# Performance work log

Hardware: AMD Instinct MI355X
Metric: run time of the kernel (lower is better)

## Reference

```python
import jax, jax.numpy as jnp
import numpy as np

# ---- quantization constants (8-bit, per-tensor affine; representative values) ----
Q_MAX = 255.0
S_IN, Z_IN = 0.05, 128.0      # block input
S1, Z1 = 0.04, 128.0          # after expand 1x1 + hardswish
S2, Z2 = 0.04, 128.0          # after depthwise 5x5 + hardswish
S_SE1, Z_SE1 = 0.03, 128.0    # SE fc1 output
S_SE2, Z_SE2 = 1.0 / 255.0, 0.0  # SE fc2 hardsigmoid output in [0,1]
S_MUL, Z_MUL = 0.04, 128.0    # SE gated activation
S3, Z3 = 0.05, 128.0          # after project 1x1
S_OUT, Z_OUT = 0.06, 128.0    # after residual add
W_SCALE = 0.01                # symmetric per-tensor weight scale (zero_point = 0)
EXP_C = 576                   # expanded channels (depthwise groups)


def conv(x, w, stride=1, padding=0, groups=1):
    return jax.lax.conv_general_dilated(
        x, w, (stride, stride), [(padding, padding), (padding, padding)],
        feature_group_count=groups, dimension_numbers=('NCHW', 'OIHW', 'NCHW'))


def hardswish(x):
    return x * jnp.clip(x + 3.0, 0.0, 6.0) * (1.0 / 6.0)


def hardsigmoid(x):
    return jnp.clip(x + 3.0, 0.0, 6.0) * (1.0 / 6.0)


def qconv(x_q, w_q, b_q, s_in, z_in, s_out, z_out, stride=1, padding=0, groups=1, act=None):
    """Quantized conv: int-domain accumulation (simulated in fp32), fused activation
    on the dequantized accumulator, then requantize to [0, Q_MAX]."""
    acc = conv(x_q - z_in, w_q, stride, padding, groups) + b_q[None, :, None, None]
    deq = acc * (s_in * W_SCALE)  # dequantize accumulator
    if act == 'hardswish':
        deq = hardswish(deq)
    elif act == 'hardsigmoid':
        deq = hardsigmoid(deq)
    return jnp.clip(deq * (1.0 / s_out) + z_out, 0.0, Q_MAX)


def setup_inputs() -> dict:
    key = jax.random.key(0)
    ks = jax.random.split(key, 11)
    def qw(k, shape):  # int8-style symmetric weights stored as fp32 integers
        return jnp.round(jnp.clip(jax.random.normal(k, shape) * 40.0, -127.0, 127.0))
    def qb(k, n):      # int32-style bias in accumulator domain
        return jnp.round(jax.random.normal(k, (n,)) * 500.0)
    return {
        'x':      jnp.round(jax.random.uniform(ks[0], (64, 96, 28, 28)) * Q_MAX),
        'w_exp':  qw(ks[1], (576, 96, 1, 1)),  'b_exp':  qb(ks[2], 576),
        'w_dw':   qw(ks[3], (576, 1, 5, 5)),   'b_dw':   qb(ks[4], 576),
        'w_se1':  qw(ks[5], (144, 576, 1, 1)), 'b_se1':  qb(ks[6], 144),
        'w_se2':  qw(ks[7], (576, 144, 1, 1)), 'b_se2':  qb(ks[8], 576),
        'w_proj': qw(ks[9], (96, 576, 1, 1)),  'b_proj': qb(ks[10], 96),
    }


def reference(x, w_exp, b_exp, w_dw, b_dw, w_se1, b_se1, w_se2, b_se2, w_proj, b_proj):
    # expand 1x1 (+ hardswish)
    e = qconv(x, w_exp, b_exp, S_IN, Z_IN, S1, Z1, act='hardswish')
    # depthwise 5x5, padding=(5-1)//2=2, groups=expanded (+ hardswish)
    d = qconv(e, w_dw, b_dw, S1, Z1, S2, Z2, padding=2, groups=EXP_C, act='hardswish')
    # squeeze-excitation: global avg pool -> fc1 -> fc2(hardsigmoid) -> quantized mul
    pooled = jnp.mean(d, axis=(2, 3), keepdims=True)  # [N, 576, 1, 1]
    g1 = qconv(pooled, w_se1, b_se1, S2, Z2, S_SE1, Z_SE1)
    g2 = qconv(g1, w_se2, b_se2, S_SE1, Z_SE1, S_SE2, Z_SE2, act='hardsigmoid')
    gated = jnp.clip((g2 - Z_SE2) * (d - Z2) * (S_SE2 * S2 / S_MUL) + Z_MUL, 0.0, Q_MAX)
    # project 1x1 (linear)
    p = qconv(gated, w_proj, b_proj, S_MUL, Z_MUL, S3, Z3)
    # quantized residual add (stride=1, in==out channels -> use_res_connect)
    out = jnp.clip((x - Z_IN) * (S_IN / S_OUT) + (p - Z3) * (S3 / S_OUT) + Z_OUT, 0.0, Q_MAX)
    return out
```

## Files before the change

### kernel.cpp

```cpp
#include <hip/hip_runtime.h>

typedef _Float16 v8h __attribute__((ext_vector_type(8)));
typedef _Float16 v4h __attribute__((ext_vector_type(4)));
typedef _Float16 v4h_a4 __attribute__((ext_vector_type(4), aligned(4)));
typedef _Float16 v2h __attribute__((ext_vector_type(2)));
typedef float v4f __attribute__((ext_vector_type(4)));

#define NB 64
#define CI 96
#define CE 576
#define CO 96
#define HW 784
#define SEC 144

#if defined(__has_builtin)
#if __has_builtin(__builtin_amdgcn_fdot2)
#define HAVE_FDOT2 1
#endif
#endif

__device__ __forceinline__ float fdot2(v2h a, v2h b, float c) {
#ifdef HAVE_FDOT2
  return __builtin_amdgcn_fdot2(a, b, c, false);
#else
  return (float)a[0] * (float)b[0] + ((float)a[1] * (float)b[1] + c);
#endif
}

__global__ __launch_bounds__(256) void k0_cvt_w(const float* __restrict__ w_exp,
                                                const float* __restrict__ w_proj,
                                                _Float16* __restrict__ w_exp_h,
                                                _Float16* __restrict__ w_proj_h) {
  int i = blockIdx.x * 256 + threadIdx.x;
  if (i < CE * CI) {
    w_exp_h[i]  = (_Float16)w_exp[i];
    w_proj_h[i] = (_Float16)w_proj[i];
  }
}

__global__ __launch_bounds__(256) void k0x_pack(const float* __restrict__ x,
                                                _Float16* __restrict__ x_f) {
  __shared__ _Float16 xl[112][104];
  const int tid = threadIdx.x;
  const int n = blockIdx.y;
  const int hw0 = blockIdx.x * 112;

  for (int idx = tid; idx < CI * 28; idx += 256) {
    int c = idx / 28, seg = idx % 28;
    const float4 v = *(const float4*)&x[(n * CI + c) * HW + hw0 + seg * 4];
    int row = seg * 4;
    xl[row + 0][c] = (_Float16)(v.x - 128.0f);
    xl[row + 1][c] = (_Float16)(v.y - 128.0f);
    xl[row + 2][c] = (_Float16)(v.z - 128.0f);
    xl[row + 3][c] = (_Float16)(v.w - 128.0f);
  }
  __syncthreads();

  for (int idx = tid; idx < 1344; idx += 256) {
    int t_l = idx / 192, rem = idx % 192, s = rem / 64, ln = rem % 64;
    int hw_l = t_l * 16 + (ln & 15), ci = s * 32 + (ln >> 4) * 8;
    v8h o;
#pragma unroll
    for (int j = 0; j < 8; ++j) o[j] = xl[hw_l][ci + j];
    size_t t = (size_t)(blockIdx.x * 7 + t_l);
    *(v8h*)&x_f[(((size_t)n * 49 + t) * 3 + s) * 512 + ln * 8] = o;
  }
}

__global__ __launch_bounds__(512, 4) void k12_fused(const _Float16* __restrict__ x_f,
                                                    const _Float16* __restrict__ w_exp_h,
                                                    const float* __restrict__ b_exp,
                                                    const float* __restrict__ w_dw,
                                                    const float* __restrict__ b_dw,
                                                    _Float16* __restrict__ d_t,
                                                    float* __restrict__ d_sums) {
  __shared__ _Float16 e_lds[16][32][36];
  __shared__ _Float16 d_tile[16][784];
  __shared__ _Float16 w_pairs[16][5][8];
  const int tid = threadIdx.x;
  const int n = blockIdx.y;
  const int c0 = blockIdx.x * 16;

  {
    unsigned long long* z = (unsigned long long*)&e_lds[0][0][0];
    for (int idx = tid; idx < 16 * 32 * 36 * 2 / 8; idx += 512) z[idx] = 0ull;
  }
  for (int idx = tid; idx < 640; idx += 512) {
    int c = idx / 40, r = idx % 40, dy = r / 8, k = r % 8;
    int tap = (k < 4) ? k : (k - 3);
    w_pairs[c][dy][k] = (_Float16)w_dw[(c0 + c) * 25 + dy * 5 + tap];
  }
  __syncthreads();

  const int wv = tid >> 6, lane = tid & 63;
  const int l15 = lane & 15, q = lane >> 4;

  {
    const _Float16* wrow = &w_exp_h[(c0 + l15) * CI + q * 8];
    v8h a0 = *(const v8h*)(wrow);
    v8h a1 = *(const v8h*)(wrow + 32);
    v8h a2 = *(const v8h*)(wrow + 64);
    float bia[4];
#pragma unroll
    for (int r = 0; r < 4; ++r) bia[r] = b_exp[c0 + q * 4 + r];

    const _Float16* xb = x_f + (size_t)n * (49 * 3 * 512) + lane * 8;
    for (int t = wv; t < 49; t += 8) {
      const _Float16* xt = xb + (size_t)t * (3 * 512);
      v8h b0 = *(const v8h*)(xt);
      v8h b1 = *(const v8h*)(xt + 512);
      v8h b2 = *(const v8h*)(xt + 1024);
      v4f acc = (v4f){0.f, 0.f, 0.f, 0.f};
      acc = __builtin_amdgcn_mfma_f32_16x16x32_f16(a0, b0, acc, 0, 0, 0);
      acc = __builtin_amdgcn_mfma_f32_16x16x32_f16(a1, b1, acc, 0, 0, 0);
      acc = __builtin_amdgcn_mfma_f32_16x16x32_f16(a2, b2, acc, 0, 0, 0);
      int hw = t * 16 + l15;
      int y = hw / 28, xx = hw - y * 28;
#pragma unroll
      for (int r = 0; r < 4; ++r) {
        float deq = (acc[r] + bia[r]) * 5.0e-4f;
        float cl  = fminf(fmaxf(deq + 3.0f, 0.0f), 6.0f);
        float ev  = fminf(fmaxf(deq * cl * (25.0f / 6.0f), -128.0f), 127.0f);
        e_lds[q * 4 + r][2 + y][6 + xx] = (_Float16)ev;
      }
    }
  }
  __syncthreads();

  const int c = tid >> 5, l = tid & 31;
  v2h W01[5], W23[5], W12[5], W34[5];
  float W0s[5], W4s[5];
#pragma unroll
  for (int dy = 0; dy < 5; ++dy) {
    W01[dy] = *(const v2h*)&w_pairs[c][dy][0];
    W23[dy] = *(const v2h*)&w_pairs[c][dy][2];
    W12[dy] = *(const v2h*)&w_pairs[c][dy][4];
    W34[dy] = *(const v2h*)&w_pairs[c][dy][6];
    W0s[dy] = (float)W01[dy][0];
    W4s[dy] = (float)W34[dy][1];
  }
  const float bc = b_dw[c0 + c];

  float csum = 0.0f;
  if (l < 28) {
    const int y = l;
    v2h P0[5], P1[5], P2[5], P3[5];
#pragma unroll
    for (int dy = 0; dy < 5; ++dy) {
      const _Float16* row = &e_lds[c][y + dy][0];
      v4h w01 = *(const v4h*)(row + 4);
      v4h w23 = *(const v4h*)(row + 8);
      P0[dy] = (v2h){w01[0], w01[1]};
      P1[dy] = (v2h){w01[2], w01[3]};
      P2[dy] = (v2h){w23[0], w23[1]};
      P3[dy] = (v2h){w23[2], w23[3]};
    }
#pragma unroll
    for (int x0 = 0; x0 < 28; x0 += 4) {
      float o0 = bc, o1 = bc, o2 = bc, o3 = bc;
#pragma unroll
      for (int dy = 0; dy < 5; ++dy) {
        o0 = fdot2(P0[dy], W01[dy], o0);
        o0 = fdot2(P1[dy], W23[dy], o0);
        o0 += (float)P2[dy][0] * W4s[dy];
        o1 += (float)P0[dy][1] * W0s[dy];
        o1 = fdot2(P1[dy], W12[dy], o1);
        o1 = fdot2(P2[dy], W34[dy], o1);
        o2 = fdot2(P1[dy], W01[dy], o2);
        o2 = fdot2(P2[dy], W23[dy], o2);
        o2 += (float)P3[dy][0] * W4s[dy];
        o3 += (float)P1[dy][1] * W0s[dy];
        o3 = fdot2(P2[dy], W12[dy], o3);
        o3 = fdot2(P3[dy], W34[dy], o3);
      }
      v4h dv;
      float oo[4] = {o0, o1, o2, o3};
#pragma unroll
      for (int i = 0; i < 4; ++i) {
        float deq = oo[i] * 4.0e-4f;
        float cl  = fminf(fmaxf(deq + 3.0f, 0.0f), 6.0f);
        float dvv = fminf(fmaxf(deq * cl * (25.0f / 6.0f), -128.0f), 127.0f);
        dv[i] = (_Float16)dvv;
        csum += dvv;
      }
      *(v4h*)&d_tile[c][y * 28 + x0] = dv;
      if (x0 < 24) {
#pragma unroll
        for (int dy = 0; dy < 5; ++dy) {
          const _Float16* row = &e_lds[c][y + dy][0];
          v4h nw = *(const v4h*)(row + x0 + 12);
          P0[dy] = P2[dy];
          P1[dy] = P3[dy];
          P2[dy] = (v2h){nw[0], nw[1]};
          P3[dy] = (v2h){nw[2], nw[3]};
        }
      }
    }
  }
#pragma unroll
  for (int m = 16; m >= 1; m >>= 1) csum += __shfl_xor(csum, m);
  if (l == 0) d_sums[n * CE + c0 + c] = csum;

  __syncthreads();
  const size_t obase = ((size_t)n * 72 + (c0 >> 3)) * 784;
  for (int hw = tid; hw < 784; hw += 512) {
    v8h o0, o1;
#pragma unroll
    for (int j = 0; j < 8; ++j) { o0[j] = d_tile[j][hw]; o1[j] = d_tile[8 + j][hw]; }
    *(v8h*)&d_t[(obase + hw) * 8] = o0;
    *(v8h*)&d_t[(obase + 784 + hw) * 8] = o1;
  }
}

__global__ __launch_bounds__(256) void k3a_fc1(const float* __restrict__ d_sums,
                                               const float* __restrict__ w_se1,
                                               const float* __restrict__ b_se1,
                                               float* __restrict__ g1) {
  const int tid = threadIdx.x;
  const int wv = tid >> 6, lane = tid & 63;
  const int n = blockIdx.y;
  const int o = blockIdx.x * 4 + wv;
  const float* wrow = &w_se1[o * CE];
  const float* srow = &d_sums[n * CE];
  float p = 0.f;
#pragma unroll
  for (int s = 0; s < 9; ++s) {
    int cc = lane + s * 64;
    p += wrow[cc] * srow[cc];
  }
#pragma unroll
  for (int m = 32; m >= 1; m >>= 1) p += __shfl_xor(p, m);
  if (lane == 0) {
    float deq = (p * (1.0f / 784.0f) + b_se1[o]) * 4.0e-4f;
    g1[n * SEC + o] = fminf(fmaxf(deq * 33.3333333f + 128.0f, 0.0f), 255.0f) - 128.0f;
  }
}

__global__ __launch_bounds__(256) void k3b_fc2(const float* __restrict__ g1,
                                               const float* __restrict__ w_se2,
                                               const float* __restrict__ b_se2,
                                               _Float16* __restrict__ g2h) {
  const int tid = threadIdx.x;
  const int wv = tid >> 6, lane = tid & 63;
  const int n = blockIdx.y;
  const int o = blockIdx.x * 4 + wv;
  const float* wrow = &w_se2[o * SEC];
  const float* grow = &g1[n * SEC];
  float p = wrow[lane] * grow[lane] + wrow[lane + 64] * grow[lane + 64];
  if (lane < 16) p += wrow[lane + 128] * grow[lane + 128];
#pragma unroll
  for (int m = 32; m >= 1; m >>= 1) p += __shfl_xor(p, m);
  if (lane == 0) {
    float deq = (p + b_se2[o]) * 3.0e-4f;
    g2h[n * CE + o] =
        (_Float16)(fminf(fmaxf(deq + 3.0f, 0.0f), 6.0f) * (1.0f / 6.0f));
  }
}

__global__ __launch_bounds__(192) void k4_proj(const _Float16* __restrict__ d_t,
                                               const _Float16* __restrict__ g2h,
                                               const _Float16* __restrict__ w_proj_h,
                                               const float* __restrict__ b_proj,
                                               const float* __restrict__ x,
                                               float* __restrict__ out) {
  const int tid = threadIdx.x;
  const int n = blockIdx.z;
  const int co0 = blockIdx.y * 48;
  const int hw0 = blockIdx.x * 112;
  const int wv = tid >> 6, lane = tid & 63;
  const int l15 = lane & 15, q = lane >> 4;

  v4f acc[7];
#pragma unroll
  for (int t = 0; t < 7; ++t) acc[t] = (v4f){0.f, 0.f, 0.f, 0.f};

  const _Float16* dbase = d_t + (((size_t)n * 72 + q) * 784 + hw0 + l15) * 8;
  const _Float16* abase = &w_proj_h[(co0 + wv * 16 + l15) * CE + q * 8];
  const _Float16* gbase = &g2h[(size_t)n * CE + q * 8];

  for (int ks = 0; ks < 18; ++ks) {
    v8h a = *(const v8h*)(abase + ks * 32);
    v8h g = *(const v8h*)(gbase + ks * 32);
    v8h ag = a * g;
    const _Float16* dk = dbase + (size_t)ks * (4 * 784 * 8);
#pragma unroll
    for (int t = 0; t < 7; ++t) {
      v8h b = *(const v8h*)(dk + t * (16 * 8));
      acc[t] = __builtin_amdgcn_mfma_f32_16x16x32_f16(ag, b, acc[t], 0, 0, 0);
    }
  }

  float bia[4];
#pragma unroll
  for (int r = 0; r < 4; ++r) bia[r] = b_proj[co0 + wv * 16 + q * 4 + r];

#pragma unroll
  for (int t = 0; t < 7; ++t) {
#pragma unroll
    for (int r = 0; r < 4; ++r) {
      int co = co0 + wv * 16 + q * 4 + r;
      int hw = hw0 + t * 16 + l15;
      float p = fminf(fmaxf((acc[t][r] + bia[r]) * 4.0e-4f * 20.0f + 128.0f, 0.0f), 255.0f);
      float xv = x[(n * CO + co) * HW + hw];
      float o = (xv - 128.0f) * 0.8333333333f + (p - 128.0f) * 0.8333333333f + 128.0f;
      out[(n * CO + co) * HW + hw] = fminf(fmaxf(o, 0.0f), 255.0f);
    }
  }
}

extern "C" void kernel_launch(void* const* d_in, const int* in_sizes, int n_in,
                              void* d_out, int out_size, void* d_ws, size_t ws_size,
                              hipStream_t stream) {
  const float* x      = (const float*)d_in[0];
  const float* w_exp  = (const float*)d_in[1];
  const float* b_exp  = (const float*)d_in[2];
  const float* w_dw   = (const float*)d_in[3];
  const float* b_dw   = (const float*)d_in[4];
  const float* w_se1  = (const float*)d_in[5];
  const float* b_se1  = (const float*)d_in[6];
  const float* w_se2  = (const float*)d_in[7];
  const float* b_se2  = (const float*)d_in[8];
  const float* w_proj = (const float*)d_in[9];
  const float* b_proj = (const float*)d_in[10];
  float* out = (float*)d_out;

  char* ws = (char*)d_ws;
  const size_t SZ_W  = (size_t)CE * CI * 2;
  const size_t SZ_XF = (size_t)NB * 49 * 3 * 512 * 2;
  const size_t SZ_D  = (size_t)NB * CE * HW * 2;
  const size_t SZ_S  = (size_t)NB * CE * 4;
  _Float16* w_exp_h  = (_Float16*)(ws);
  _Float16* w_proj_h = (_Float16*)(ws + SZ_W);
  _Float16* x_f      = (_Float16*)(ws + 2 * SZ_W);
  _Float16* d_t      = (_Float16*)(ws + 2 * SZ_W + SZ_XF);
  float*    d_sums   = (float*)   (ws + 2 * SZ_W + SZ_XF + SZ_D);
  float*    g1       = (float*)   (ws + 2 * SZ_W + SZ_XF + SZ_D + SZ_S);
  _Float16* g2h      = (_Float16*)(ws + 2 * SZ_W + SZ_XF + SZ_D + 2 * SZ_S);

  k0_cvt_w<<<(CE * CI + 255) / 256, 256, 0, stream>>>(w_exp, w_proj, w_exp_h, w_proj_h);
  k0x_pack<<<dim3(7, NB), 256, 0, stream>>>(x, x_f);
  k12_fused<<<dim3(36, NB), 512, 0, stream>>>(x_f, w_exp_h, b_exp, w_dw, b_dw, d_t, d_sums);
  k3a_fc1<<<dim3(36, NB), 256, 0, stream>>>(d_sums, w_se1, b_se1, g1);
  k3b_fc2<<<dim3(144, NB), 256, 0, stream>>>(g1, w_se2, b_se2, g2h);
  k4_proj<<<dim3(7, 2, NB), 192, 0, stream>>>(d_t, g2h, w_proj_h, b_proj, x, out);
}
```

Baseline: 179.5 us.

## Split fused expand+depthwise kernel into two spatial halves with halo recompute

The fused expand-1x1 plus depthwise-5x5 kernel now splits each image into two 14-row halves, one per block. Each block recomputes the expand output for a 2-row halo, which the tile loop covers as 28 of the 49 tiles. Smaller LDS tiles and launch bounds raised to 8 blocks/CU aim to double block count and improve occupancy. Per-half channel sums go to a doubled buffer that fc1 adds together. In exchange, about 14% of the expand MFMA work is redundant and the depthwise loop has an irregular tail.

```diff
diff --git a/kernel.cpp b/kernel.cpp
--- a/kernel.cpp
+++ b/kernel.cpp
@@ -2,7 +2,6 @@
 
 typedef _Float16 v8h __attribute__((ext_vector_type(8)));
 typedef _Float16 v4h __attribute__((ext_vector_type(4)));
-typedef _Float16 v4h_a4 __attribute__((ext_vector_type(4), aligned(4)));
 typedef _Float16 v2h __attribute__((ext_vector_type(2)));
 typedef float v4f __attribute__((ext_vector_type(4)));
 
@@ -67,23 +66,24 @@
   }
 }
 
-__global__ __launch_bounds__(512, 4) void k12_fused(const _Float16* __restrict__ x_f,
+__global__ __launch_bounds__(512, 8) void k12_fused(const _Float16* __restrict__ x_f,
                                                     const _Float16* __restrict__ w_exp_h,
                                                     const float* __restrict__ b_exp,
                                                     const float* __restrict__ w_dw,
                                                     const float* __restrict__ b_dw,
                                                     _Float16* __restrict__ d_t,
-                                                    float* __restrict__ d_sums) {
-  __shared__ _Float16 e_lds[16][32][36];
-  __shared__ _Float16 d_tile[16][784];
+                                                    float* __restrict__ d_sums2) {
+  __shared__ _Float16 e_lds[16][18][38];
+  __shared__ _Float16 d_tile[16][392];
   __shared__ _Float16 w_pairs[16][5][8];
   const int tid = threadIdx.x;
-  const int n = blockIdx.y;
+  const int n = blockIdx.z;
+  const int h = blockIdx.y;
   const int c0 = blockIdx.x * 16;
 
   {
     unsigned long long* z = (unsigned long long*)&e_lds[0][0][0];
-    for (int idx = tid; idx < 16 * 32 * 36 * 2 / 8; idx += 512) z[idx] = 0ull;
+    for (int idx = tid; idx < 16 * 18 * 38 * 2 / 8; idx += 512) z[idx] = 0ull;
   }
   for (int idx = tid; idx < 640; idx += 512) {
     int c = idx / 40, r = idx % 40, dy = r / 8, k = r % 8;
@@ -104,8 +104,10 @@
 #pragma unroll
     for (int r = 0; r < 4; ++r) bia[r] = b_exp[c0 + q * 4 + r];
 
+    const int ir0 = 14 * h - 2;
     const _Float16* xb = x_f + (size_t)n * (49 * 3 * 512) + lane * 8;
-    for (int t = wv; t < 49; t += 8) {
+    for (int t_l = wv; t_l < 28; t_l += 8) {
+      int t = 21 * h + t_l;
       const _Float16* xt = xb + (size_t)t * (3 * 512);
       v8h b0 = *(const v8h*)(xt);
       v8h b1 = *(const v8h*)(xt + 512);
@@ -116,12 +118,13 @@
       acc = __builtin_amdgcn_mfma_f32_16x16x32_f16(a2, b2, acc, 0, 0, 0);
       int hw = t * 16 + l15;
       int y = hw / 28, xx = hw - y * 28;
+      int r_l = y - ir0;
 #pragma unroll
       for (int r = 0; r < 4; ++r) {
         float deq = (acc[r] + bia[r]) * 5.0e-4f;
         float cl  = fminf(fmaxf(deq + 3.0f, 0.0f), 6.0f);
         float ev  = fminf(fmaxf(deq * cl * (25.0f / 6.0f), -128.0f), 127.0f);
-        e_lds[q * 4 + r][2 + y][6 + xx] = (_Float16)ev;
+        e_lds[q * 4 + r][r_l][6 + xx] = (_Float16)ev;
       }
     }
   }
@@ -143,20 +146,20 @@
 
   float csum = 0.0f;
   if (l < 28) {
-    const int y = l;
+    const int ry = l >> 1;
+    const int bx = (l & 1) * 14;
     v2h P0[5], P1[5], P2[5], P3[5];
 #pragma unroll
     for (int dy = 0; dy < 5; ++dy) {
-      const _Float16* row = &e_lds[c][y + dy][0];
-      v4h w01 = *(const v4h*)(row + 4);
-      v4h w23 = *(const v4h*)(row + 8);
-      P0[dy] = (v2h){w01[0], w01[1]};
-      P1[dy] = (v2h){w01[2], w01[3]};
-      P2[dy] = (v2h){w23[0], w23[1]};
-      P3[dy] = (v2h){w23[2], w23[3]};
-    }
-#pragma unroll
-    for (int x0 = 0; x0 < 28; x0 += 4) {
+      const _Float16* row = &e_lds[c][ry + dy][bx];
+      P0[dy] = *(const v2h*)(row + 4);
+      P1[dy] = *(const v2h*)(row + 6);
+      P2[dy] = *(const v2h*)(row + 8);
+      P3[dy] = *(const v2h*)(row + 10);
+    }
+#pragma unroll
+    for (int xi = 0; xi < 3; ++xi) {
+      const int x0 = bx + xi * 4;
       float o0 = bc, o1 = bc, o2 = bc, o3 = bc;
 #pragma unroll
       for (int dy = 0; dy < 5; ++dy) {
@@ -173,46 +176,68 @@
         o3 = fdot2(P2[dy], W12[dy], o3);
         o3 = fdot2(P3[dy], W34[dy], o3);
       }
-      v4h dv;
       float oo[4] = {o0, o1, o2, o3};
+      v2h dva, dvb;
 #pragma unroll
       for (int i = 0; i < 4; ++i) {
+        float deq = oo[i] * 4.0e-4f;
+        float cl  = fminf(fmaxf(deq + 3.0f, 0.0f), 6.0f);
+        float dvv = fminf(fmaxf(deq * cl * (25.0f / 6.0f), -128.0f), 127.0f);
+        if (i < 2) dva[i] = (_Float16)dvv; else dvb[i - 2] = (_Float16)dvv;
+        csum += dvv;
+      }
+      *(v2h*)&d_tile[c][ry * 28 + x0]     = dva;
+      *(v2h*)&d_tile[c][ry * 28 + x0 + 2] = dvb;
+#pragma unroll
+      for (int dy = 0; dy < 5; ++dy) {
+        const _Float16* row = &e_lds[c][ry + dy][bx];
+        P0[dy] = P2[dy];
+        P1[dy] = P3[dy];
+        P2[dy] = *(const v2h*)(row + x0 - bx + 12);
+        P3[dy] = *(const v2h*)(row + x0 - bx + 14);
+      }
+    }
+    {
+      float o0 = bc, o1 = bc;
+#pragma unroll
+      for (int dy = 0; dy < 5; ++dy) {
+        o0 = fdot2(P0[dy], W01[dy], o0);
+        o0 = fdot2(P1[dy], W23[dy], o0);
+        o0 += (float)P2[dy][0] * W4s[dy];
+        o1 += (float)P0[dy][1] * W0s[dy];
+        o1 = fdot2(P1[dy], W12[dy], o1);
+        o1 = fdot2(P2[dy], W34[dy], o1);
+      }
+      v2h dv;
+      float oo[2] = {o0, o1};
+#pragma unroll
+      for (int i = 0; i < 2; ++i) {
         float deq = oo[i] * 4.0e-4f;
         float cl  = fminf(fmaxf(deq + 3.0f, 0.0f), 6.0f);
         float dvv = fminf(fmaxf(deq * cl * (25.0f / 6.0f), -128.0f), 127.0f);
         dv[i] = (_Float16)dvv;
         csum += dvv;
       }
-      *(v4h*)&d_tile[c][y * 28 + x0] = dv;
-      if (x0 < 24) {
-#pragma unroll
-        for (int dy = 0; dy < 5; ++dy) {
-          const _Float16* row = &e_lds[c][y + dy][0];
-          v4h nw = *(const v4h*)(row + x0 + 12);
-          P0[dy] = P2[dy];
-          P1[dy] = P3[dy];
-          P2[dy] = (v2h){nw[0], nw[1]};
-          P3[dy] = (v2h){nw[2], nw[3]};
-        }
-      }
+      *(v2h*)&d_tile[c][ry * 28 + bx + 12] = dv;
     }
   }
 #pragma unroll
   for (int m = 16; m >= 1; m >>= 1) csum += __shfl_xor(csum, m);
-  if (l == 0) d_sums[n * CE + c0 + c] = csum;
+  if (l == 0) d_sums2[((size_t)h * NB + n) * CE + c0 + c] = csum;
 
   __syncthreads();
-  const size_t obase = ((size_t)n * 72 + (c0 >> 3)) * 784;
-  for (int hw = tid; hw < 784; hw += 512) {
+  const size_t obase = ((size_t)n * 72 + (c0 >> 3)) * 784 + 392 * h;
+  if (tid < 392) {
+    int hw_l = tid;
     v8h o0, o1;
 #pragma unroll
-    for (int j = 0; j < 8; ++j) { o0[j] = d_tile[j][hw]; o1[j] = d_tile[8 + j][hw]; }
-    *(v8h*)&d_t[(obase + hw) * 8] = o0;
-    *(v8h*)&d_t[(obase + 784 + hw) * 8] = o1;
-  }
-}
-
-__global__ __launch_bounds__(256) void k3a_fc1(const float* __restrict__ d_sums,
+    for (int j = 0; j < 8; ++j) { o0[j] = d_tile[j][hw_l]; o1[j] = d_tile[8 + j][hw_l]; }
+    *(v8h*)&d_t[(obase + hw_l) * 8] = o0;
+    *(v8h*)&d_t[(obase + 784 + hw_l) * 8] = o1;
+  }
+}
+
+__global__ __launch_bounds__(256) void k3a_fc1(const float* __restrict__ d_sums2,
                                                const float* __restrict__ w_se1,
                                                const float* __restrict__ b_se1,
                                                float* __restrict__ g1) {
@@ -221,12 +246,13 @@
   const int n = blockIdx.y;
   const int o = blockIdx.x * 4 + wv;
   const float* wrow = &w_se1[o * CE];
-  const float* srow = &d_sums[n * CE];
+  const float* s0 = &d_sums2[(size_t)n * CE];
+  const float* s1 = &d_sums2[((size_t)NB + n) * CE];
   float p = 0.f;
 #pragma unroll
   for (int s = 0; s < 9; ++s) {
     int cc = lane + s * 64;
-    p += wrow[cc] * srow[cc];
+    p += wrow[cc] * (s0[cc] + s1[cc]);
   }
 #pragma unroll
   for (int m = 32; m >= 1; m >>= 1) p += __shfl_xor(p, m);
@@ -328,19 +354,20 @@
   const size_t SZ_W  = (size_t)CE * CI * 2;
   const size_t SZ_XF = (size_t)NB * 49 * 3 * 512 * 2;
   const size_t SZ_D  = (size_t)NB * CE * HW * 2;
+  const size_t SZ_S2 = (size_t)2 * NB * CE * 4;
   const size_t SZ_S  = (size_t)NB * CE * 4;
   _Float16* w_exp_h  = (_Float16*)(ws);
   _Float16* w_proj_h = (_Float16*)(ws + SZ_W);
   _Float16* x_f      = (_Float16*)(ws + 2 * SZ_W);
   _Float16* d_t      = (_Float16*)(ws + 2 * SZ_W + SZ_XF);
-  float*    d_sums   = (float*)   (ws + 2 * SZ_W + SZ_XF + SZ_D);
-  float*    g1       = (float*)   (ws + 2 * SZ_W + SZ_XF + SZ_D + SZ_S);
-  _Float16* g2h      = (_Float16*)(ws + 2 * SZ_W + SZ_XF + SZ_D + 2 * SZ_S);
+  float*    d_sums2  = (float*)   (ws + 2 * SZ_W + SZ_XF + SZ_D);
+  float*    g1       = (float*)   (ws + 2 * SZ_W + SZ_XF + SZ_D + SZ_S2);
+  _Float16* g2h      = (_Float16*)(ws + 2 * SZ_W + SZ_XF + SZ_D + SZ_S2 + SZ_S);
 
   k0_cvt_w<<<(CE * CI + 255) / 256, 256, 0, stream>>>(w_exp, w_proj, w_exp_h, w_proj_h);
   k0x_pack<<<dim3(7, NB), 256, 0, stream>>>(x, x_f);
-  k12_fused<<<dim3(36, NB), 512, 0, stream>>>(x_f, w_exp_h, b_exp, w_dw, b_dw, d_t, d_sums);
-  k3a_fc1<<<dim3(36, NB), 256, 0, stream>>>(d_sums, w_se1, b_se1, g1);
+  k12_fused<<<dim3(36, 2, NB), 512, 0, stream>>>(x_f, w_exp_h, b_exp, w_dw, b_dw, d_t, d_sums2);
+  k3a_fc1<<<dim3(36, NB), 256, 0, stream>>>(d_sums2, w_se1, b_se1, g1);
   k3b_fc2<<<dim3(144, NB), 256, 0, stream>>>(g1, w_se2, b_se2, g2h);
   k4_proj<<<dim3(7, 2, NB), 192, 0, stream>>>(d_t, g2h, w_proj_h, b_proj, x, out);
 }
```

Result: faster. 175.6 us (-2.2%).
